# Kernel tuning notes

Hardware: AMD Instinct MI355X
Metric: run time of the kernel (lower is better)

## Reference

```python
import jax, jax.numpy as jnp
import numpy as np

B, N, C = 2, 2048, 768
H = 12
HD = C // H  # 64


def setup_inputs() -> dict:
    key = jax.random.key(0)
    ks = jax.random.split(key, 6)
    s = 0.02
    x = jax.random.normal(ks[0], (B, N, C), dtype=jnp.float32)
    xpos = jnp.arange(B * N, dtype=jnp.int64).reshape(B, N) % N
    W_qkv = jax.random.normal(ks[1], (3 * C, C), dtype=jnp.float32) * s
    b_qkv = jnp.zeros((3 * C,), dtype=jnp.float32)
    W_proj = jax.random.normal(ks[2], (C, C), dtype=jnp.float32) * s
    b_proj = jnp.zeros((C,), dtype=jnp.float32)
    return {"x": x, "xpos": xpos, "W_qkv": W_qkv, "b_qkv": b_qkv,
            "W_proj": W_proj, "b_proj": b_proj}


def reference(x, xpos, W_qkv, b_qkv, W_proj, b_proj):
    # rope is None in this configuration -> xpos is unused, matching torch module.
    Bx, Nx, Cx = x.shape
    scale = (Cx // H) ** -0.5
    qkv = x @ W_qkv.T + b_qkv                     # [B, N, 3C]
    qkv = qkv.reshape(Bx, Nx, 3, H, HD)
    q = jnp.einsum('bnhd->bhnd', qkv[:, :, 0])    # [B, H, N, HD]
    k = jnp.einsum('bnhd->bhnd', qkv[:, :, 1])
    v = jnp.einsum('bnhd->bhnd', qkv[:, :, 2])
    attn = jnp.einsum('bhnd,bhmd->bhnm', q, k) * scale  # [B, H, N, N]
    attn = jax.nn.softmax(attn, axis=-1)
    out = jnp.einsum('bhnm,bhmd->bhnd', attn, v)  # [B, H, N, HD]
    out = jnp.einsum('bhnd->bnhd', out).reshape(Bx, Nx, Cx)
    return out @ W_proj.T + b_proj
```

## Files before the change

### kernel.cpp

```cpp
#include <hip/hip_runtime.h>
#include <hip/hip_bf16.h>


typedef _Float16 half8 __attribute__((ext_vector_type(8)));
typedef _Float16 half4_t __attribute__((ext_vector_type(4)));
typedef float floatx4 __attribute__((ext_vector_type(4)));

#define LDA 72
#define LDP 72
#define SCALE_LOG2E 0.1803368801111204f

constexpr int XH_OFF    = 0;
constexpr int WQKV_OFF  = XH_OFF + 4096 * 768;
constexpr int WPROJ_OFF = WQKV_OFF + 2304 * 768;
constexpr int QK_OFF    = WPROJ_OFF + 768 * 768;
constexpr int VTH_OFF   = QK_OFF + 4096 * 1536;
constexpr int PO_OFF    = VTH_OFF + 24 * 64 * 2048;
constexpr int PSTAT_OFF = PO_OFF + 2 * 24 * 2048 * 64;

__device__ __forceinline__ void gl16(const _Float16* g, _Float16* l) {
  __builtin_amdgcn_global_load_lds(
      (const __attribute__((address_space(1))) unsigned int*)g,
      (__attribute__((address_space(3))) unsigned int*)l, 16, 0, 0);
}

__global__ __launch_bounds__(256) void cvt_all(const float* __restrict__ x,
                                               const float* __restrict__ wqkv,
                                               const float* __restrict__ wproj,
                                               _Float16* __restrict__ ws) {
  constexpr int n1 = 4096 * 768 / 4;
  constexpr int n2 = 2304 * 768 / 4;
  int i = blockIdx.x * 256 + threadIdx.x;
  const float* src; _Float16* dst; int j;
  if (i < n1)           { src = x;     dst = ws + XH_OFF;    j = i; }
  else if (i < n1 + n2) { src = wqkv;  dst = ws + WQKV_OFF;  j = i - n1; }
  else                  { src = wproj; dst = ws + WPROJ_OFF; j = i - n1 - n2; }
  floatx4 f = *(const floatx4*)(src + 4 * j);
  half4_t h;
  h[0] = (_Float16)f[0]; h[1] = (_Float16)f[1];
  h[2] = (_Float16)f[2]; h[3] = (_Float16)f[3];
  *(half4_t*)(dst + 4 * j) = h;
}

__global__ __launch_bounds__(256) void qkv_gemm(const _Float16* __restrict__ xh,
                                                const _Float16* __restrict__ wh,
                                                const float* __restrict__ bias,
                                                _Float16* __restrict__ qkh,
                                                _Float16* __restrict__ vth) {
  __shared__ __align__(16) _Float16 sA[64 * 64];
  __shared__ __align__(16) _Float16 sB[128 * 64];
  const int tid = threadIdx.x;
  const int nblk = blockIdx.x % 18, mblk = blockIdx.x / 18;
  const int lane = tid & 63, w = tid >> 6;
  const int lane15 = lane & 15, quad = lane >> 4;
  const int lrow = lane >> 3, lchunk = lane & 7;

  floatx4 acc[4][2];
#pragma unroll
  for (int mt = 0; mt < 4; ++mt)
#pragma unroll
    for (int nt = 0; nt < 2; ++nt) acc[mt][nt] = (floatx4){0.f, 0.f, 0.f, 0.f};

  for (int kt = 0; kt < 12; ++kt) {
    if (kt) __syncthreads();
#pragma unroll
    for (int i = 0; i < 6; ++i) {
      int g = w * 48 + 8 * i;
      if (g < 64)
        gl16(xh + (mblk * 64 + g + lrow) * 768 + kt * 64 + lchunk * 8, sA + g * 64);
      else
        gl16(wh + (nblk * 128 + (g - 64) + lrow) * 768 + kt * 64 + lchunk * 8,
             sB + (g - 64) * 64);
    }
    __syncthreads();
#pragma unroll
    for (int ks = 0; ks < 2; ++ks) {
      half8 af[4], bf[2];
#pragma unroll
      for (int mt = 0; mt < 4; ++mt)
        af[mt] = *(const half8*)(sA + (mt * 16 + lane15) * 64 + ks * 32 + quad * 8);
#pragma unroll
      for (int nt = 0; nt < 2; ++nt)
        bf[nt] = *(const half8*)(sB + (w * 32 + nt * 16 + lane15) * 64 + ks * 32 + quad * 8);
#pragma unroll
      for (int mt = 0; mt < 4; ++mt)
#pragma unroll
        for (int nt = 0; nt < 2; ++nt)
          acc[mt][nt] = __builtin_amdgcn_mfma_f32_16x16x32_f16(af[mt], bf[nt], acc[mt][nt], 0, 0, 0);
    }
  }

  const int mbase = mblk * 64;
#pragma unroll
  for (int nt = 0; nt < 2; ++nt) {
    int cbase = nblk * 128 + w * 32 + nt * 16;
    float bv = bias[cbase + lane15];
    if (cbase < 1536) {
      int col = cbase + lane15;
      float sc = (cbase < 768) ? SCALE_LOG2E : 1.0f;
#pragma unroll
      for (int mt = 0; mt < 4; ++mt)
#pragma unroll
        for (int r = 0; r < 4; ++r) {
          int token = mbase + mt * 16 + quad * 4 + r;
          qkh[token * 1536 + col] = (_Float16)((acc[mt][nt][r] + bv) * sc);
        }
    } else {
      int dcol = cbase - 1536 + lane15;
      int h = dcol >> 6, d = dcol & 63;
#pragma unroll
      for (int mt = 0; mt < 4; ++mt) {
        int tok0 = mbase + mt * 16 + quad * 4;
        int b = tok0 >> 11, n0 = tok0 & 2047;
        int bh = b * 12 + h;
        half4_t hv;
#pragma unroll
        for (int r = 0; r < 4; ++r) hv[r] = (_Float16)(acc[mt][nt][r] + bv);
        *(half4_t*)(vth + (bh * 64 + d) * 2048 + n0) = hv;
      }
    }
  }
}

__global__ __launch_bounds__(512) void attn_fused(const _Float16* __restrict__ qkh,
                                                  const _Float16* __restrict__ vth,
                                                  _Float16* __restrict__ pO,
                                                  float* __restrict__ pM,
                                                  float* __restrict__ pL) {
  __shared__ __align__(16) _Float16 sK[64 * LDA];
  __shared__ __align__(16) _Float16 sVT[64 * LDA];
  __shared__ __align__(16) _Float16 sP[8 * 16 * LDP];
  const int tid = threadIdx.x;
  const int bx = blockIdx.x;
  const int bh = bx % 24;
  const int rest = bx / 24;
  const int ks = rest & 1, qt = rest >> 1;
  const int b = bh / 12, h = bh % 12;
  const int lane = tid & 63, w = tid >> 6;
  const int lane15 = lane & 15, quad = lane >> 4;
  const int chunk = tid & 7, rbase = tid >> 3;
  const int wq = w >> 2, ww = w & 3;
  _Float16* sPw = sP + w * 16 * LDP;

  const int qkbase = b * 2048 * 1536 + h * 64;
  const int qrow = qt * 128 + wq * 64 + ww * 16 + lane15;
  half8 qa0 = *(const half8*)(qkh + qkbase + qrow * 1536 + quad * 8);
  half8 qa1 = *(const half8*)(qkh + qkbase + qrow * 1536 + 32 + quad * 8);

  const _Float16* kptr = qkh + qkbase + 768;
  const _Float16* vptr = vth + bh * 64 * 2048;

  floatx4 O[4];
#pragma unroll
  for (int dt = 0; dt < 4; ++dt) O[dt] = (floatx4){0.f, 0.f, 0.f, 0.f};
  float mrow = -3.0e38f, lrow = 0.f;

  const int kt0 = ks * 16;
  for (int kt = kt0; kt < kt0 + 16; ++kt) {
    half8 tk = *(const half8*)(kptr + (kt * 64 + rbase) * 1536 + chunk * 8);
    half8 tv = *(const half8*)(vptr + rbase * 2048 + kt * 64 + chunk * 8);
    if (kt != kt0) __syncthreads();
    *(half8*)(sK + rbase * LDA + chunk * 8) = tk;
    *(half8*)(sVT + rbase * LDA + chunk * 8) = tv;
    __syncthreads();

    floatx4 s[4];
#pragma unroll
    for (int nt = 0; nt < 4; ++nt) {
      half8 kf0 = *(const half8*)(sK + (nt * 16 + lane15) * LDA + quad * 8);
      half8 kf1 = *(const half8*)(sK + (nt * 16 + lane15) * LDA + 32 + quad * 8);
      floatx4 a = (floatx4){0.f, 0.f, 0.f, 0.f};
      a = __builtin_amdgcn_mfma_f32_16x16x32_f16(kf0, qa0, a, 0, 0, 0);
      a = __builtin_amdgcn_mfma_f32_16x16x32_f16(kf1, qa1, a, 0, 0, 0);
      s[nt] = a;
    }

    float tmax = s[0][0];
#pragma unroll
    for (int nt = 0; nt < 4; ++nt)
#pragma unroll
      for (int r = 0; r < 4; ++r) tmax = fmaxf(tmax, s[nt][r]);
    tmax = fmaxf(tmax, __shfl_xor(tmax, 16, 64));
    tmax = fmaxf(tmax, __shfl_xor(tmax, 32, 64));

    if (__any(tmax > mrow)) {
      float mnew = fmaxf(mrow, tmax);
      float alpha = exp2f(mrow - mnew);
      lrow *= alpha;
      mrow = mnew;
      float ar[4];
#pragma unroll
      for (int r = 0; r < 4; ++r) ar[r] = __shfl(alpha, 4 * quad + r, 64);
#pragma unroll
      for (int dt = 0; dt < 4; ++dt)
#pragma unroll
        for (int r = 0; r < 4; ++r) O[dt][r] *= ar[r];
    }

    float rsum = 0.f;
#pragma unroll
    for (int nt = 0; nt < 4; ++nt)
#pragma unroll
      for (int r = 0; r < 4; ++r) {
        float p = exp2f(s[nt][r] - mrow);
        s[nt][r] = p;
        rsum += p;
      }
    rsum += __shfl_xor(rsum, 16, 64);
    rsum += __shfl_xor(rsum, 32, 64);
    lrow += rsum;

#pragma unroll
    for (int nt = 0; nt < 4; ++nt) {
      half4_t hp;
#pragma unroll
      for (int r = 0; r < 4; ++r) hp[r] = (_Float16)s[nt][r];
      *(half4_t*)(sPw + lane15 * LDP + nt * 16 + quad * 4) = hp;
    }
    asm volatile("s_waitcnt lgkmcnt(0)" ::: "memory");

#pragma unroll
    for (int kk = 0; kk < 2; ++kk) {
      half8 pa = *(const half8*)(sPw + lane15 * LDP + kk * 32 + quad * 8);
#pragma unroll
      for (int dt = 0; dt < 4; ++dt) {
        half8 vb = *(const half8*)(sVT + (dt * 16 + lane15) * LDA + kk * 32 + quad * 8);
        O[dt] = __builtin_amdgcn_mfma_f32_16x16x32_f16(pa, vb, O[dt], 0, 0, 0);
      }
    }
  }

  const int prow = (ks * 24 + bh) * 2048 + qt * 128 + wq * 64 + ww * 16;
#pragma unroll
  for (int dt = 0; dt < 4; ++dt)
#pragma unroll
    for (int r = 0; r < 4; ++r)
      pO[(prow + quad * 4 + r) * 64 + dt * 16 + lane15] = (_Float16)O[dt][r];
  if (lane < 16) {
    pM[prow + lane] = mrow;
    pL[prow + lane] = lrow;
  }
}

__global__ __launch_bounds__(256) void attn_merge(const _Float16* __restrict__ pO,
                                                  const float* __restrict__ pM,
                                                  const float* __restrict__ pL,
                                                  _Float16* __restrict__ aoh) {
  int gid = blockIdx.x * 256 + threadIdx.x;
  int row = gid >> 3, chunk = gid & 7;
  int bh = row >> 11, tok = row & 2047;
  float m1 = pM[row], l1 = pL[row];
  float m2 = pM[49152 + row], l2 = pL[49152 + row];
  float M = fmaxf(m1, m2);
  float f1 = exp2f(m1 - M), f2 = exp2f(m2 - M);
  float inv = 1.0f / (f1 * l1 + f2 * l2);
  f1 *= inv; f2 *= inv;
  half8 o1 = *(const half8*)(pO + row * 64 + chunk * 8);
  half8 o2 = *(const half8*)(pO + 3145728 + row * 64 + chunk * 8);
  half8 o;
#pragma unroll
  for (int e = 0; e < 8; ++e)
    o[e] = (_Float16)(f1 * (float)o1[e] + f2 * (float)o2[e]);
  int b = bh / 12, h = bh % 12;
  *(half8*)(aoh + (b * 2048 + tok) * 768 + h * 64 + chunk * 8) = o;
}

__global__ __launch_bounds__(256) void proj_gemm(const _Float16* __restrict__ ah,
                                                 const _Float16* __restrict__ wh,
                                                 const float* __restrict__ bias,
                                                 float* __restrict__ out) {
  __shared__ __align__(16) _Float16 sA[64 * 64];
  __shared__ __align__(16) _Float16 sB[128 * 64];
  const int tid = threadIdx.x;
  const int nblk = blockIdx.x % 6, mblk = blockIdx.x / 6;
  const int lane = tid & 63, w = tid >> 6;
  const int lane15 = lane & 15, quad = lane >> 4;
  const int lrow = lane >> 3, lchunk = lane & 7;

  floatx4 acc[4][2];
#pragma unroll
  for (int mt = 0; mt < 4; ++mt)
#pragma unroll
    for (int nt = 0; nt < 2; ++nt) acc[mt][nt] = (floatx4){0.f, 0.f, 0.f, 0.f};

  for (int kt = 0; kt < 12; ++kt) {
    if (kt) __syncthreads();
#pragma unroll
    for (int i = 0; i < 6; ++i) {
      int g = w * 48 + 8 * i;
      if (g < 64)
        gl16(ah + (mblk * 64 + g + lrow) * 768 + kt * 64 + lchunk * 8, sA + g * 64);
      else
        gl16(wh + (nblk * 128 + (g - 64) + lrow) * 768 + kt * 64 + lchunk * 8,
             sB + (g - 64) * 64);
    }
    __syncthreads();
#pragma unroll
    for (int ks = 0; ks < 2; ++ks) {
      half8 af[4], bf[2];
#pragma unroll
      for (int mt = 0; mt < 4; ++mt)
        af[mt] = *(const half8*)(sA + (mt * 16 + lane15) * 64 + ks * 32 + quad * 8);
#pragma unroll
      for (int nt = 0; nt < 2; ++nt)
        bf[nt] = *(const half8*)(sB + (w * 32 + nt * 16 + lane15) * 64 + ks * 32 + quad * 8);
#pragma unroll
      for (int mt = 0; mt < 4; ++mt)
#pragma unroll
        for (int nt = 0; nt < 2; ++nt)
          acc[mt][nt] = __builtin_amdgcn_mfma_f32_16x16x32_f16(af[mt], bf[nt], acc[mt][nt], 0, 0, 0);
    }
  }

  const int mbase = mblk * 64;
#pragma unroll
  for (int nt = 0; nt < 2; ++nt) {
    int col = nblk * 128 + w * 32 + nt * 16 + lane15;
    float bv = bias[col];
#pragma unroll
    for (int mt = 0; mt < 4; ++mt)
#pragma unroll
      for (int r = 0; r < 4; ++r) {
        int token = mbase + mt * 16 + quad * 4 + r;
        out[token * 768 + col] = acc[mt][nt][r] + bv;
      }
  }
}

extern "C" void kernel_launch(void* const* d_in, const int* in_sizes, int n_in,
                              void* d_out, int out_size, void* d_ws, size_t ws_size,
                              hipStream_t stream) {
  const float* x     = (const float*)d_in[0];
  const float* wqkv  = (const float*)d_in[2];
  const float* bqkv  = (const float*)d_in[3];
  const float* wproj = (const float*)d_in[4];
  const float* bproj = (const float*)d_in[5];
  float* out = (float*)d_out;

  _Float16* ws = (_Float16*)d_ws;
  _Float16* xh     = ws + XH_OFF;
  _Float16* wqkvh  = ws + WQKV_OFF;
  _Float16* wprojh = ws + WPROJ_OFF;
  _Float16* qkh    = ws + QK_OFF;
  _Float16* vth    = ws + VTH_OFF;
  _Float16* pO     = ws + PO_OFF;
  float*    pM     = (float*)(ws + PSTAT_OFF);
  float*    pL     = pM + 2 * 49152;
  _Float16* aoh    = xh;

  constexpr int total_v4 = (4096 * 768 + 2304 * 768 + 768 * 768) / 4;
  cvt_all<<<total_v4 / 256, 256, 0, stream>>>(x, wqkv, wproj, ws);
  qkv_gemm<<<64 * 18, 256, 0, stream>>>(xh, wqkvh, bqkv, qkh, vth);
  attn_fused<<<24 * 32, 512, 0, stream>>>(qkh, vth, pO, pM, pL);
  attn_merge<<<1536, 256, 0, stream>>>(pO, pM, pL, aoh);
  proj_gemm<<<64 * 6, 256, 0, stream>>>(aoh, wprojh, bproj, out);
}
```

Measured before the change: 188.4 us.

## Fuse split-K attention merge into projection GEMM and prefetch K/V tiles

Removes the separate attn_merge kernel by having proj_gemm combine the two split-K partial attention outputs while it loads its A tile into shared memory. This saves one launch and the write and re-read of the merged attention buffer. In exchange, each projection block recomputes the merge for its rows once per column block, so six times in total, and the A-tile load becomes a plain register load instead of an async global-to-LDS copy. Separately, the attention loop now prefetches the next K/V tile into registers after the barrier, so global loads overlap with the compute.

```diff
diff --git a/kernel.cpp b/kernel.cpp
--- a/kernel.cpp
+++ b/kernel.cpp
@@ -155,14 +155,19 @@
   for (int dt = 0; dt < 4; ++dt) O[dt] = (floatx4){0.f, 0.f, 0.f, 0.f};
   float mrow = -3.0e38f, lrow = 0.f;
 
-  const int kt0 = ks * 16;
-  for (int kt = kt0; kt < kt0 + 16; ++kt) {
-    half8 tk = *(const half8*)(kptr + (kt * 64 + rbase) * 1536 + chunk * 8);
-    half8 tv = *(const half8*)(vptr + rbase * 2048 + kt * 64 + chunk * 8);
+  const int kt0 = ks * 16, ktend = kt0 + 16;
+  half8 tk = *(const half8*)(kptr + (kt0 * 64 + rbase) * 1536 + chunk * 8);
+  half8 tv = *(const half8*)(vptr + rbase * 2048 + kt0 * 64 + chunk * 8);
+
+  for (int kt = kt0; kt < ktend; ++kt) {
     if (kt != kt0) __syncthreads();
     *(half8*)(sK + rbase * LDA + chunk * 8) = tk;
     *(half8*)(sVT + rbase * LDA + chunk * 8) = tv;
     __syncthreads();
+    if (kt + 1 < ktend) {
+      tk = *(const half8*)(kptr + ((kt + 1) * 64 + rbase) * 1536 + chunk * 8);
+      tv = *(const half8*)(vptr + rbase * 2048 + (kt + 1) * 64 + chunk * 8);
+    }
 
     floatx4 s[4];
 #pragma unroll
@@ -242,40 +247,22 @@
   }
 }
 
-__global__ __launch_bounds__(256) void attn_merge(const _Float16* __restrict__ pO,
-                                                  const float* __restrict__ pM,
-                                                  const float* __restrict__ pL,
-                                                  _Float16* __restrict__ aoh) {
-  int gid = blockIdx.x * 256 + threadIdx.x;
-  int row = gid >> 3, chunk = gid & 7;
-  int bh = row >> 11, tok = row & 2047;
-  float m1 = pM[row], l1 = pL[row];
-  float m2 = pM[49152 + row], l2 = pL[49152 + row];
-  float M = fmaxf(m1, m2);
-  float f1 = exp2f(m1 - M), f2 = exp2f(m2 - M);
-  float inv = 1.0f / (f1 * l1 + f2 * l2);
-  f1 *= inv; f2 *= inv;
-  half8 o1 = *(const half8*)(pO + row * 64 + chunk * 8);
-  half8 o2 = *(const half8*)(pO + 3145728 + row * 64 + chunk * 8);
-  half8 o;
-#pragma unroll
-  for (int e = 0; e < 8; ++e)
-    o[e] = (_Float16)(f1 * (float)o1[e] + f2 * (float)o2[e]);
-  int b = bh / 12, h = bh % 12;
-  *(half8*)(aoh + (b * 2048 + tok) * 768 + h * 64 + chunk * 8) = o;
-}
-
-__global__ __launch_bounds__(256) void proj_gemm(const _Float16* __restrict__ ah,
+__global__ __launch_bounds__(256) void proj_gemm(const _Float16* __restrict__ pO,
+                                                 const float* __restrict__ pM,
+                                                 const float* __restrict__ pL,
                                                  const _Float16* __restrict__ wh,
                                                  const float* __restrict__ bias,
                                                  float* __restrict__ out) {
-  __shared__ __align__(16) _Float16 sA[64 * 64];
+  __shared__ __align__(16) _Float16 sA[64 * 72];
   __shared__ __align__(16) _Float16 sB[128 * 64];
   const int tid = threadIdx.x;
   const int nblk = blockIdx.x % 6, mblk = blockIdx.x / 6;
   const int lane = tid & 63, w = tid >> 6;
   const int lane15 = lane & 15, quad = lane >> 4;
   const int lrow = lane >> 3, lchunk = lane & 7;
+  const int arow = tid >> 2, achk = tid & 3;
+  const int tok0 = mblk * 64;
+  const int b = tok0 >> 11, tokl = tok0 & 2047;
 
   floatx4 acc[4][2];
 #pragma unroll
@@ -284,26 +271,44 @@
     for (int nt = 0; nt < 2; ++nt) acc[mt][nt] = (floatx4){0.f, 0.f, 0.f, 0.f};
 
   for (int kt = 0; kt < 12; ++kt) {
+    const int bh = b * 12 + kt;
+    const int row1 = bh * 2048 + tokl + arow;
+    const int row2 = (24 + bh) * 2048 + tokl + arow;
+    float m1 = pM[row1], l1 = pL[row1];
+    float m2 = pM[row2], l2 = pL[row2];
+    float M = fmaxf(m1, m2);
+    float f1 = exp2f(m1 - M), f2 = exp2f(m2 - M);
+    float inv = 1.0f / (f1 * l1 + f2 * l2);
+    f1 *= inv; f2 *= inv;
+
     if (kt) __syncthreads();
 #pragma unroll
-    for (int i = 0; i < 6; ++i) {
-      int g = w * 48 + 8 * i;
-      if (g < 64)
-        gl16(ah + (mblk * 64 + g + lrow) * 768 + kt * 64 + lchunk * 8, sA + g * 64);
-      else
-        gl16(wh + (nblk * 128 + (g - 64) + lrow) * 768 + kt * 64 + lchunk * 8,
-             sB + (g - 64) * 64);
+    for (int i = 0; i < 4; ++i) {
+      int g = w * 32 + 8 * i;
+      gl16(wh + (nblk * 128 + g + lrow) * 768 + kt * 64 + lchunk * 8, sB + g * 64);
+    }
+#pragma unroll
+    for (int cc = 0; cc < 2; ++cc) {
+      int c8 = achk + 4 * cc;
+      half8 o1 = *(const half8*)(pO + row1 * 64 + c8 * 8);
+      half8 o2 = *(const half8*)(pO + row2 * 64 + c8 * 8);
+      half8 o;
+#pragma unroll
+      for (int e = 0; e < 8; ++e)
+        o[e] = (_Float16)(f1 * (float)o1[e] + f2 * (float)o2[e]);
+      *(half8*)(sA + arow * 72 + c8 * 8) = o;
     }
     __syncthreads();
-#pragma unroll
-    for (int ks = 0; ks < 2; ++ks) {
+
+#pragma unroll
+    for (int ksplit = 0; ksplit < 2; ++ksplit) {
       half8 af[4], bf[2];
 #pragma unroll
       for (int mt = 0; mt < 4; ++mt)
-        af[mt] = *(const half8*)(sA + (mt * 16 + lane15) * 64 + ks * 32 + quad * 8);
+        af[mt] = *(const half8*)(sA + (mt * 16 + lane15) * 72 + ksplit * 32 + quad * 8);
 #pragma unroll
       for (int nt = 0; nt < 2; ++nt)
-        bf[nt] = *(const half8*)(sB + (w * 32 + nt * 16 + lane15) * 64 + ks * 32 + quad * 8);
+        bf[nt] = *(const half8*)(sB + (w * 32 + nt * 16 + lane15) * 64 + ksplit * 32 + quad * 8);
 #pragma unroll
       for (int mt = 0; mt < 4; ++mt)
 #pragma unroll
@@ -346,12 +351,10 @@
   _Float16* pO     = ws + PO_OFF;
   float*    pM     = (float*)(ws + PSTAT_OFF);
   float*    pL     = pM + 2 * 49152;
-  _Float16* aoh    = xh;
 
   constexpr int total_v4 = (4096 * 768 + 2304 * 768 + 768 * 768) / 4;
   cvt_all<<<total_v4 / 256, 256, 0, stream>>>(x, wqkv, wproj, ws);
   qkv_gemm<<<64 * 18, 256, 0, stream>>>(xh, wqkvh, bqkv, qkh, vth);
   attn_fused<<<24 * 32, 512, 0, stream>>>(qkh, vth, pO, pM, pL);
-  attn_merge<<<1536, 256, 0, stream>>>(pO, pM, pL, aoh);
-  proj_gemm<<<64 * 6, 256, 0, stream>>>(aoh, wprojh, bproj, out);
-}
+  proj_gemm<<<64 * 6, 256, 0, stream>>>(pO, pM, pL, wprojh, bproj, out);
+}
```

Measured after the change: 192.5 us. 1.02x slower.
